# Kernel tuning notes

Hardware: AMD Instinct MI355X
Metric: run time of the kernel (lower is better)

The kernel has to match this reference:

```python
import jax, jax.numpy as jnp
import numpy as np

N_CH = 62
F_DIM = 16
T_DIM = 32
B_DIM = 256
N_NODES = B_DIM * N_CH  # 15872
E_DIM = 200000
SEQ = T_DIM * F_DIM  # 512


def setup_inputs() -> dict:
    key = jax.random.key(0)
    ks = iter(jax.random.split(key, 40))
    s = 0.05
    inp = {}
    inp['x'] = jax.random.normal(next(ks), (N_NODES, F_DIM, T_DIM), dtype=jnp.float32)
    inp['edge_index'] = jax.random.randint(next(ks), (T_DIM, 2, E_DIM), 0, N_NODES, dtype=jnp.int64)
    inp['edge_weight'] = jax.random.uniform(next(ks), (T_DIM, E_DIM), dtype=jnp.float32)
    inp['batch'] = jax.random.randint(next(ks), (T_DIM, N_NODES), 0, B_DIM, dtype=jnp.int64)
    # ChebConv params (K=2): lins have no bias, single bias added at end
    for p in ['c1', 'c2']:
        inp[p + '_w0'] = jax.random.normal(next(ks), (F_DIM, F_DIM), dtype=jnp.float32) * s
        inp[p + '_w1'] = jax.random.normal(next(ks), (F_DIM, F_DIM), dtype=jnp.float32) * s
        inp[p + '_b'] = jnp.zeros((F_DIM,), jnp.float32)
    # LSTM params (torch gate order i,f,g,o); fold b_ih+b_hh into one bias
    for name, i_dim, h_dim in [('l1', N_CH, 64), ('l2', 64, 128), ('l3', 128, 256)]:
        inp[name + '_wih'] = jax.random.normal(next(ks), (4 * h_dim, i_dim), dtype=jnp.float32) * s
        inp[name + '_whh'] = jax.random.normal(next(ks), (4 * h_dim, h_dim), dtype=jnp.float32) * s
        inp[name + '_b'] = jnp.zeros((4 * h_dim,), jnp.float32)
    # MLP head
    for name, i_dim, o_dim in [('fc1', SEQ * 256, 256), ('fc2', 256, 128), ('fc3', 128, 64), ('fc4', 64, 4)]:
        inp[name + '_w'] = jax.random.normal(next(ks), (i_dim, o_dim), dtype=jnp.float32) * s
        inp[name + '_b'] = jnp.zeros((o_dim,), jnp.float32)
    return inp


def _cheb(x, src, dst, w, w0, w1, b):
    # PyG ChebConv K=2, sym norm, lambda_max=2: Tx1 = -D^{-1/2} A D^{-1/2} x
    n = x.shape[0]
    deg = jax.ops.segment_sum(w, src, num_segments=n)
    dinv = jnp.where(deg > 0, jax.lax.rsqrt(deg), 0.0)
    norm = -dinv[src] * w * dinv[dst]
    tx1 = jax.ops.segment_sum(norm[:, None] * x[src], dst, num_segments=n)
    return x @ w0 + tx1 @ w1 + b


def _lstm(x, wih, whh, b):
    # x: [B, S, I] -> [B, S, H], batch_first, zero init state
    bsz, _, _ = x.shape
    h_dim = whh.shape[1]
    xg = x @ wih.T + b  # precompute input gates [B, S, 4H]
    def step(carry, xt):
        h, c = carry
        g = xt + h @ whh.T
        i, f, gg, o = jnp.split(g, 4, axis=-1)
        c = jax.nn.sigmoid(f) * c + jax.nn.sigmoid(i) * jnp.tanh(gg)
        h = jax.nn.sigmoid(o) * jnp.tanh(c)
        return (h, c), h
    h0 = jnp.zeros((bsz, h_dim), x.dtype)
    _, hs = jax.lax.scan(step, (h0, h0), jnp.swapaxes(xg, 0, 1))
    return jnp.swapaxes(hs, 0, 1)


def reference(x, edge_index, edge_weight, batch,
              c1_w0, c1_w1, c1_b, c2_w0, c2_w1, c2_b,
              l1_wih, l1_whh, l1_b, l2_wih, l2_whh, l2_b, l3_wih, l3_whh, l3_b,
              fc1_w, fc1_b, fc2_w, fc2_b, fc3_w, fc3_b, fc4_w, fc4_b):
    def per_t(xt, ei, w):
        h = _cheb(xt, ei[0], ei[1], w, c1_w0, c1_w1, c1_b)
        h = jax.nn.leaky_relu(h, 0.01)
        return _cheb(h, ei[0], ei[1], w, c2_w0, c2_w1, c2_b)
    xt_first = jnp.moveaxis(x, -1, 0)  # [T, N, F]
    h = jax.vmap(per_t)(xt_first, edge_index, edge_weight)  # [T, N, F]
    xc = jnp.moveaxis(h, 0, -1)  # [N, F, T]
    xc = xc.reshape(B_DIM, N_CH, F_DIM, T_DIM)
    xc = jnp.transpose(xc, (0, 3, 2, 1))  # [B, T, F, 62]
    xc = xc.reshape(B_DIM, T_DIM * F_DIM, N_CH)  # [B, S, 62]
    h = _lstm(xc, l1_wih, l1_whh, l1_b)
    h = _lstm(h, l2_wih, l2_whh, l2_b)
    h = _lstm(h, l3_wih, l3_whh, l3_b)
    z = h.reshape(B_DIM, -1)  # [B, S*256]
    z = jax.nn.relu(z @ fc1_w + fc1_b)
    z = jax.nn.relu(z @ fc2_w + fc2_b)
    z = jax.nn.relu(z @ fc3_w + fc3_b)
    return z @ fc4_w + fc4_b
```

## Files before the change

kernel.cpp:

```cpp
#include <hip/hip_runtime.h>
#include <cstdint>
#include <cstddef>


#define T_DIM 32
#define F_DIMC 16
#define NNODE 15872
#define EDGES 200000
#define BATCH 256
#define SEQL 512
#define TN (T_DIM * NNODE)
#define TE (T_DIM * EDGES)

typedef unsigned short ushortT;
typedef __bf16 bf16_t;
typedef bf16_t bf16x8 __attribute__((ext_vector_type(8)));
typedef float f32x4 __attribute__((ext_vector_type(4)));

__device__ __forceinline__ ushortT f2bf(float f) {
  union { float f; unsigned u; } v; v.f = f;
  unsigned u = v.u;
  u += 0x7fffu + ((u >> 16) & 1u);
  return (ushortT)(u >> 16);
}
__device__ __forceinline__ float fsig(float x) { return 1.0f / (1.0f + __expf(-x)); }
__device__ __forceinline__ float ftanh(float x) {
  float e = __expf(2.0f * x);
  return 1.0f - 2.0f / (e + 1.0f);
}
#define PIN(v) asm volatile("" : "+v"(v))

__device__ __forceinline__ void bar_sync() {
  asm volatile("s_waitcnt lgkmcnt(0)\n\ts_barrier" ::: "memory");
  __builtin_amdgcn_sched_barrier(0);
}

__global__ void k_wprep(const float* __restrict__ w1i, const float* __restrict__ w1h,
                        const float* __restrict__ w2i, const float* __restrict__ w2h,
                        const float* __restrict__ w3i, const float* __restrict__ w3h,
                        ushortT* __restrict__ Wcat) {
  int id = blockIdx.x * 256 + threadIdx.x;
  if (id >= 524288) return;
  float v;
  if (id < 32768) {
    int g = id >> 7, k = id & 127;
    v = (k < 62) ? w1i[g * 62 + k] : ((k >= 64) ? w1h[g * 64 + (k - 64)] : 0.0f);
  } else if (id < 131072) {
    int j = id - 32768; int g = j / 192, k = j % 192;
    v = (k < 64) ? w2i[g * 64 + k] : w2h[g * 128 + (k - 64)];
  } else {
    int j = id - 131072; int g = j / 384, k = j % 384;
    v = (k < 128) ? w3i[g * 128 + k] : w3h[g * 256 + (k - 128)];
  }
  Wcat[id] = f2bf(v);
}

__global__ void k_transpose(const float* __restrict__ x, float* __restrict__ xt) {
  __shared__ float s[528];
  int n = blockIdx.x;
  int tid = threadIdx.x;
  for (int i = tid; i < 512; i += 256) {
    s[(i >> 5) * 33 + (i & 31)] = x[(size_t)n * 512 + i];
  }
  __syncthreads();
  for (int i = tid; i < 512; i += 256) {
    int t = i >> 4, f = i & 15;
    xt[((size_t)t * NNODE + n) * 16 + f] = s[f * 33 + t];
  }
}

__global__ void k_degcount(const int* __restrict__ ei, const float* __restrict__ ew,
                           float* __restrict__ deg, int* __restrict__ counts) {
  int id = blockIdx.x * 256 + threadIdx.x;
  if (id >= TE) return;
  int t = id / EDGES, e = id % EDGES;
  int src = ei[(2 * t) * EDGES + e];
  int dst = ei[(2 * t + 1) * EDGES + e];
  atomicAdd(&deg[t * NNODE + src], ew[id]);
  atomicAdd(&counts[t * NNODE + dst], 1);
}

__global__ void k_scanA(const int* __restrict__ counts, int* __restrict__ offs,
                        int* __restrict__ ctot, float* __restrict__ deg) {
  __shared__ int s[256];
  int tid = threadIdx.x;
  int gid = blockIdx.x * 256 + tid;
  float d = deg[gid];
  int v = counts[gid];
  s[tid] = v; __syncthreads();
  for (int off = 1; off < 256; off <<= 1) {
    int x = (tid >= off) ? s[tid - off] : 0;
    __syncthreads();
    s[tid] += x;
    __syncthreads();
  }
  offs[gid] = s[tid] - v;
  if (tid == 255) ctot[blockIdx.x] = s[255];
  deg[gid] = (d > 0.0f) ? rsqrtf(d) : 0.0f;
}

__global__ void k_scanB(const int* __restrict__ ctot, int* __restrict__ cbase) {
  __shared__ int s[256];
  int tid = threadIdx.x;
  int carry = 0;
  for (int c = 0; c < 8; ++c) {
    int i = c * 256 + tid;
    int v = (i < 1984) ? ctot[i] : 0;
    s[tid] = v; __syncthreads();
    for (int off = 1; off < 256; off <<= 1) {
      int x = (tid >= off) ? s[tid - off] : 0;
      __syncthreads();
      s[tid] += x;
      __syncthreads();
    }
    if (i < 1984) cbase[i] = carry + s[tid] - v;
    int tot = s[255];
    __syncthreads();
    carry += tot;
  }
}

__global__ void k_fill(const int* __restrict__ ei, const float* __restrict__ ew,
                       const float* __restrict__ dinv, const int* __restrict__ offs,
                       const int* __restrict__ cbase, int* __restrict__ fillc,
                       int* __restrict__ csrs, float* __restrict__ csrn) {
  int id = blockIdx.x * 256 + threadIdx.x;
  if (id >= TE) return;
  int t = id / EDGES, e = id % EDGES;
  int src = ei[(2 * t) * EDGES + e];
  int dst = ei[(2 * t + 1) * EDGES + e];
  int idx = t * NNODE + dst;
  int pos = offs[idx] + cbase[idx >> 8] + atomicAdd(&fillc[idx], 1);
  csrs[pos] = src;
  csrn[pos] = -dinv[t * NNODE + src] * ew[id] * dinv[idx];
}

__device__ __forceinline__ void fma4(float4& a, float sc, const float4 b) {
  a.x += sc * b.x; a.y += sc * b.y; a.z += sc * b.z; a.w += sc * b.w;
}

__global__ void k_gc(const float* __restrict__ in, const int* __restrict__ offs,
                     const int* __restrict__ cbase,
                     const int* __restrict__ csrs, const float* __restrict__ csrn,
                     const float* __restrict__ w0, const float* __restrict__ w1,
                     const float* __restrict__ bias, float* __restrict__ outF,
                     ushortT* __restrict__ outX, int mode) {
  __shared__ float sw0[256], sw1[256], sb[16];
  int tid = threadIdx.x;
  sw0[tid] = w0[tid];
  sw1[tid] = w1[tid];
  if (tid < 16) sb[tid] = bias[tid];
  __syncthreads();
  int idx = blockIdx.x * 256 + tid;
  if (idx >= TN) return;
  int t = idx / NNODE, n = idx % NNODE;
  const float4* rowp = (const float4*)(in + (size_t)idx * 16);
  float4 x0 = rowp[0], x1 = rowp[1], x2 = rowp[2], x3 = rowp[3];
  float4 a0 = {0, 0, 0, 0}, a1 = {0, 0, 0, 0}, a2 = {0, 0, 0, 0}, a3 = {0, 0, 0, 0};
  int beg = offs[idx] + cbase[idx >> 8];
  int end = (idx == TN - 1) ? TE : offs[idx + 1] + cbase[(idx + 1) >> 8];
  const float* base = in + (size_t)t * NNODE * 16;
  for (int p2 = beg; p2 < end; ++p2) {
    int s = csrs[p2];
    float nr = csrn[p2];
    const float4* rp = (const float4*)(base + (size_t)s * 16);
    fma4(a0, nr, rp[0]); fma4(a1, nr, rp[1]); fma4(a2, nr, rp[2]); fma4(a3, nr, rp[3]);
  }
  float xr[16], ar[16];
  *(float4*)&xr[0] = x0; *(float4*)&xr[4] = x1; *(float4*)&xr[8] = x2; *(float4*)&xr[12] = x3;
  *(float4*)&ar[0] = a0; *(float4*)&ar[4] = a1; *(float4*)&ar[8] = a2; *(float4*)&ar[12] = a3;
  float o[16];
#pragma unroll
  for (int j = 0; j < 16; ++j) o[j] = sb[j];
#pragma unroll
  for (int k = 0; k < 16; ++k) {
    float xv = xr[k], av = ar[k];
#pragma unroll
    for (int j = 0; j < 16; ++j) o[j] += xv * sw0[k * 16 + j] + av * sw1[k * 16 + j];
  }
  if (mode == 0) {
#pragma unroll
    for (int j = 0; j < 16; ++j) o[j] = (o[j] > 0.0f) ? o[j] : 0.01f * o[j];
    float4* op = (float4*)(outF + (size_t)idx * 16);
    op[0] = *(float4*)&o[0]; op[1] = *(float4*)&o[4];
    op[2] = *(float4*)&o[8]; op[3] = *(float4*)&o[12];
  } else {
    int bb = n / 62, ch = n % 62;
#pragma unroll
    for (int j = 0; j < 16; ++j)
      outX[((size_t)(bb * 512 + t * 16 + j)) * 64 + ch] = f2bf(o[j]);
    if (ch < 2) {
#pragma unroll
      for (int j = 0; j < 16; ++j)
        outX[((size_t)(bb * 512 + t * 16 + j)) * 64 + 62 + ch] = 0;
    }
  }
}

__global__ __launch_bounds__(512, 1) void k_lstm(const ushortT* __restrict__ xc,
                                                 const ushortT* __restrict__ Wcat,
                                                 const float* __restrict__ b1g,
                                                 const float* __restrict__ b2g,
                                                 const float* __restrict__ b3g,
                                                 ushortT* __restrict__ zbuf,
                                                 uint32_t* __restrict__ h2x,
                                                 uint32_t* __restrict__ xbuf) {
  __shared__ ushortT X1[2][16 * 72];
  __shared__ ushortT H1[2][16 * 72];
  __shared__ ushortT H2[2][16 * 136];
  __shared__ ushortT HS[2][16 * 136];
  __shared__ ushortT PS[2][16 * 136];
  __shared__ ushortT H2S[2][16 * 136];
  int tid = threadIdx.x;
  int wv = tid >> 6, lane = tid & 63;
  int col = lane & 15, koff = (lane >> 4) * 8, m = lane & 15;
  int bx = blockIdx.x;

  if (bx < 16) {
    int g = bx;
    int bg = g * 16;
    const ushortT* W1 = Wcat;
    const ushortT* W2 = Wcat + 32768;

    bf16x8 w1r[4][4];
    if (wv < 4) {
#pragma unroll
      for (int q = 0; q < 4; ++q)
#pragma unroll
        for (int k = 0; k < 4; ++k) {
          w1r[q][k] = *reinterpret_cast<const bf16x8*>(
              &W1[(size_t)(q * 64 + wv * 16 + col) * 128 + k * 32 + koff]);
          PIN(w1r[q][k]);
        }
    }
    bf16x8 w2r[4][6];
#pragma unroll
    for (int q = 0; q < 4; ++q)
#pragma unroll
      for (int k = 0; k < 6; ++k) {
        w2r[q][k] = *reinterpret_cast<const bf16x8*>(
            &W2[(size_t)(q * 128 + wv * 16 + col) * 192 + k * 32 + koff]);
        PIN(w2r[q][k]);
      }
    float b1v[4] = {0, 0, 0, 0}, b2v[4];
    if (wv < 4) {
#pragma unroll
      for (int q = 0; q < 4; ++q) b1v[q] = b1g[q * 64 + wv * 16 + col];
    }
#pragma unroll
    for (int q = 0; q < 4; ++q) b2v[q] = b2g[q * 128 + wv * 16 + col];

    float c1r[4] = {0, 0, 0, 0};
    float c2r[4] = {0, 0, 0, 0};

    for (int i = tid; i < 2 * 16 * 72; i += 512) { X1[0][i] = 0; H1[0][i] = 0; }
    for (int i = tid; i < 2 * 16 * 136; i += 512) H2[0][i] = 0;
    __syncthreads();
    uint4 xreg = {0, 0, 0, 0};
    {
      int tid2 = tid - 256;
      if (tid2 >= 0 && tid2 < 128) {
        int mm = tid2 >> 3, jj = (tid2 & 7) * 8;
        *(uint4*)&X1[0][mm * 72 + jj] =
            *(const uint4*)&xc[((size_t)(bg + mm) * 512 + 0) * 64 + jj];
        xreg = *(const uint4*)&xc[((size_t)(bg + mm) * 512 + 1) * 64 + jj];
      }
    }
    __syncthreads();

    uint32_t* h2g = h2x + (size_t)g * 512 * 2048;

    for (int t = 0; t < 512; ++t) {
      int pr = t & 1, pw = 1 - pr;
      if (wv < 4) {
        f32x4 acc[4] = {};
#pragma unroll
        for (int kt = 0; kt < 4; ++kt) {
          const ushortT* ap = (kt < 2) ? &X1[pr][m * 72 + kt * 32 + koff]
                                       : &H1[pr][m * 72 + (kt - 2) * 32 + koff];
          bf16x8 a = *reinterpret_cast<const bf16x8*>(ap);
#pragma unroll
          for (int q = 0; q < 4; ++q)
            acc[q] = __builtin_amdgcn_mfma_f32_16x16x32_bf16(a, w1r[q][kt], acc[q], 0, 0, 0);
        }
#pragma unroll
        for (int r = 0; r < 4; ++r) {
          int row = (lane >> 4) * 4 + r;
          int lc = wv * 16 + col;
          float gi = acc[0][r] + b1v[0];
          float gf = acc[1][r] + b1v[1];
          float gg = acc[2][r] + b1v[2];
          float go = acc[3][r] + b1v[3];
          float c = fsig(gf) * c1r[r] + fsig(gi) * ftanh(gg);
          float h = fsig(go) * ftanh(c);
          c1r[r] = c;
          H1[pw][row * 72 + lc] = f2bf(h);
        }
      } else {
        int tid2 = tid - 256;
        if (tid2 < 128) {
          int mm = tid2 >> 3, jj = (tid2 & 7) * 8;
          if (t + 1 < 512)
            *(uint4*)&X1[pw][mm * 72 + jj] = xreg;
          int tf = (t + 2 < 512) ? t + 2 : 511;
          xreg = *(const uint4*)&xc[((size_t)(bg + mm) * 512 + tf) * 64 + jj];
        }
      }
      bar_sync();
      {
        f32x4 acc[4] = {};
#pragma unroll
        for (int kt = 0; kt < 6; ++kt) {
          const ushortT* ap = (kt < 2) ? &H1[pw][m * 72 + kt * 32 + koff]
                                       : &H2[pr][m * 136 + (kt - 2) * 32 + koff];
          bf16x8 a = *reinterpret_cast<const bf16x8*>(ap);
#pragma unroll
          for (int q = 0; q < 4; ++q)
            acc[q] = __builtin_amdgcn_mfma_f32_16x16x32_bf16(a, w2r[q][kt], acc[q], 0, 0, 0);
        }
        uint32_t tag = ((uint32_t)(t + 1)) << 16;
#pragma unroll
        for (int r = 0; r < 4; ++r) {
          int row = (lane >> 4) * 4 + r;
          int lc = wv * 16 + col;
          float gi = acc[0][r] + b2v[0];
          float gf = acc[1][r] + b2v[1];
          float gg = acc[2][r] + b2v[2];
          float go = acc[3][r] + b2v[3];
          float c = fsig(gf) * c2r[r] + fsig(gi) * ftanh(gg);
          float h = fsig(go) * ftanh(c);
          c2r[r] = c;
          ushortT hb = f2bf(h);
          H2[pw][row * 136 + lc] = hb;
          __hip_atomic_store(&h2g[(size_t)t * 2048 + row * 128 + lc], tag | hb,
                             __ATOMIC_RELAXED, __HIP_MEMORY_SCOPE_AGENT);
        }
      }
      bar_sync();
    }
  } else {
    int bxx = bx - 16;
    int s = (bxx >> 3) & 1;
    int g = (bxx & 7) | ((bxx >> 4) << 3);
    int ps = 1 - s;
    int bg = g * 16;
    const ushortT* W3 = Wcat + 131072;

    bf16x8 wH[4][4], wO[4][4], wP[4][4];
#pragma unroll
    for (int q = 0; q < 4; ++q) {
      const ushortT* rw = &W3[(size_t)(q * 256 + s * 128 + wv * 16 + col) * 384];
#pragma unroll
      for (int j = 0; j < 4; ++j) {
        wH[q][j] = *reinterpret_cast<const bf16x8*>(&rw[j * 32 + koff]);
        wO[q][j] = *reinterpret_cast<const bf16x8*>(&rw[(4 + s * 4 + j) * 32 + koff]);
        wP[q][j] = *reinterpret_cast<const bf16x8*>(&rw[(4 + ps * 4 + j) * 32 + koff]);
        PIN(wH[q][j]); PIN(wO[q][j]); PIN(wP[q][j]);
      }
    }
    float b3v[4];
#pragma unroll
    for (int q = 0; q < 4; ++q) b3v[q] = b3g[q * 256 + s * 128 + wv * 16 + col];

    float c3r[4] = {0, 0, 0, 0};

    for (int i = tid; i < 2 * 16 * 136; i += 512) HS[0][i] = 0;
    __syncthreads();

    uint32_t* myslot = xbuf + (((size_t)g * 2 + s) * 2) * 2048;
    const uint32_t* pslot = xbuf + (((size_t)g * 2 + ps) * 2) * 2048;
    const uint32_t* h2g = h2x + (size_t)g * 512 * 2048;

    int prow = tid >> 5, pc0 = (tid & 31) * 4;

    {
      const uint32_t* hp = h2g + prow * 128 + pc0;
      uint32_t u0 = __hip_atomic_load(hp + 0, __ATOMIC_RELAXED, __HIP_MEMORY_SCOPE_AGENT);
      uint32_t u1 = __hip_atomic_load(hp + 1, __ATOMIC_RELAXED, __HIP_MEMORY_SCOPE_AGENT);
      uint32_t u2 = __hip_atomic_load(hp + 2, __ATOMIC_RELAXED, __HIP_MEMORY_SCOPE_AGENT);
      uint32_t u3 = __hip_atomic_load(hp + 3, __ATOMIC_RELAXED, __HIP_MEMORY_SCOPE_AGENT);
      for (;;) {
        bool ok = ((u0 >> 16) == 1u) & ((u1 >> 16) == 1u) &
                  ((u2 >> 16) == 1u) & ((u3 >> 16) == 1u);
        if (ok) break;
        u0 = __hip_atomic_load(hp + 0, __ATOMIC_RELAXED, __HIP_MEMORY_SCOPE_AGENT);
        u1 = __hip_atomic_load(hp + 1, __ATOMIC_RELAXED, __HIP_MEMORY_SCOPE_AGENT);
        u2 = __hip_atomic_load(hp + 2, __ATOMIC_RELAXED, __HIP_MEMORY_SCOPE_AGENT);
        u3 = __hip_atomic_load(hp + 3, __ATOMIC_RELAXED, __HIP_MEMORY_SCOPE_AGENT);
      }
      H2S[0][prow * 136 + pc0 + 0] = (ushortT)(u0 & 0xffffu);
      H2S[0][prow * 136 + pc0 + 1] = (ushortT)(u1 & 0xffffu);
      H2S[0][prow * 136 + pc0 + 2] = (ushortT)(u2 & 0xffffu);
      H2S[0][prow * 136 + pc0 + 3] = (ushortT)(u3 & 0xffffu);
    }
    __syncthreads();

    for (int t = 0; t < 512; ++t) {
      int prt = t & 1, pw = 1 - prt;
      const uint32_t* pb = pslot + (size_t)prt * 2048 + prow * 128 + pc0;
      uint32_t v0 = 0, v1 = 0, v2 = 0, v3 = 0;
      if (t > 0) {
        v0 = __hip_atomic_load(pb + 0, __ATOMIC_RELAXED, __HIP_MEMORY_SCOPE_AGENT);
        v1 = __hip_atomic_load(pb + 1, __ATOMIC_RELAXED, __HIP_MEMORY_SCOPE_AGENT);
        v2 = __hip_atomic_load(pb + 2, __ATOMIC_RELAXED, __HIP_MEMORY_SCOPE_AGENT);
        v3 = __hip_atomic_load(pb + 3, __ATOMIC_RELAXED, __HIP_MEMORY_SCOPE_AGENT);
      }
      const uint32_t* hp = h2g + (size_t)(t + 1) * 2048 + prow * 128 + pc0;
      uint32_t u0 = 0, u1 = 0, u2 = 0, u3 = 0;
      if (t < 511) {
        u0 = __hip_atomic_load(hp + 0, __ATOMIC_RELAXED, __HIP_MEMORY_SCOPE_AGENT);
        u1 = __hip_atomic_load(hp + 1, __ATOMIC_RELAXED, __HIP_MEMORY_SCOPE_AGENT);
        u2 = __hip_atomic_load(hp + 2, __ATOMIC_RELAXED, __HIP_MEMORY_SCOPE_AGENT);
        u3 = __hip_atomic_load(hp + 3, __ATOMIC_RELAXED, __HIP_MEMORY_SCOPE_AGENT);
      }
      __builtin_amdgcn_sched_barrier(0);
      f32x4 acc[4] = {};
#pragma unroll
      for (int kt = 0; kt < 4; ++kt) {
        bf16x8 a = *reinterpret_cast<const bf16x8*>(&H2S[prt][m * 136 + kt * 32 + koff]);
#pragma unroll
        for (int q = 0; q < 4; ++q)
          acc[q] = __builtin_amdgcn_mfma_f32_16x16x32_bf16(a, wH[q][kt], acc[q], 0, 0, 0);
      }
      if (t > 0) {
#pragma unroll
        for (int j = 0; j < 4; ++j) {
          bf16x8 a = *reinterpret_cast<const bf16x8*>(&HS[prt][m * 136 + j * 32 + koff]);
#pragma unroll
          for (int q = 0; q < 4; ++q)
            acc[q] = __builtin_amdgcn_mfma_f32_16x16x32_bf16(a, wO[q][j], acc[q], 0, 0, 0);
        }
        {
          uint32_t want = (uint32_t)t;
          while (((v0 >> 16) != want) | ((v1 >> 16) != want) |
                 ((v2 >> 16) != want) | ((v3 >> 16) != want)) {
            v0 = __hip_atomic_load(pb + 0, __ATOMIC_RELAXED, __HIP_MEMORY_SCOPE_AGENT);
            v1 = __hip_atomic_load(pb + 1, __ATOMIC_RELAXED, __HIP_MEMORY_SCOPE_AGENT);
            v2 = __hip_atomic_load(pb + 2, __ATOMIC_RELAXED, __HIP_MEMORY_SCOPE_AGENT);
            v3 = __hip_atomic_load(pb + 3, __ATOMIC_RELAXED, __HIP_MEMORY_SCOPE_AGENT);
          }
          PS[prt][prow * 136 + pc0 + 0] = (ushortT)(v0 & 0xffffu);
          PS[prt][prow * 136 + pc0 + 1] = (ushortT)(v1 & 0xffffu);
          PS[prt][prow * 136 + pc0 + 2] = (ushortT)(v2 & 0xffffu);
          PS[prt][prow * 136 + pc0 + 3] = (ushortT)(v3 & 0xffffu);
        }
        bar_sync();
#pragma unroll
        for (int j = 0; j < 4; ++j) {
          bf16x8 a = *reinterpret_cast<const bf16x8*>(&PS[prt][m * 136 + j * 32 + koff]);
#pragma unroll
          for (int q = 0; q < 4; ++q)
            acc[q] = __builtin_amdgcn_mfma_f32_16x16x32_bf16(a, wP[q][j], acc[q], 0, 0, 0);
        }
      }
      if (t < 511) {
        uint32_t want = (uint32_t)(t + 2);
        while (((u0 >> 16) != want) | ((u1 >> 16) != want) |
               ((u2 >> 16) != want) | ((u3 >> 16) != want)) {
          u0 = __hip_atomic_load(hp + 0, __ATOMIC_RELAXED, __HIP_MEMORY_SCOPE_AGENT);
          u1 = __hip_atomic_load(hp + 1, __ATOMIC_RELAXED, __HIP_MEMORY_SCOPE_AGENT);
          u2 = __hip_atomic_load(hp + 2, __ATOMIC_RELAXED, __HIP_MEMORY_SCOPE_AGENT);
          u3 = __hip_atomic_load(hp + 3, __ATOMIC_RELAXED, __HIP_MEMORY_SCOPE_AGENT);
        }
        H2S[pw][prow * 136 + pc0 + 0] = (ushortT)(u0 & 0xffffu);
        H2S[pw][prow * 136 + pc0 + 1] = (ushortT)(u1 & 0xffffu);
        H2S[pw][prow * 136 + pc0 + 2] = (ushortT)(u2 & 0xffffu);
        H2S[pw][prow * 136 + pc0 + 3] = (ushortT)(u3 & 0xffffu);
      }
      uint32_t* mw = myslot + (size_t)((t + 1) & 1) * 2048;
      ushortT hbs[4];
#pragma unroll
      for (int r = 0; r < 4; ++r) {
        int row = (lane >> 4) * 4 + r;
        int lc = wv * 16 + col;
        float gi = acc[0][r] + b3v[0];
        float gf = acc[1][r] + b3v[1];
        float gg = acc[2][r] + b3v[2];
        float go = acc[3][r] + b3v[3];
        float c = fsig(gf) * c3r[r] + fsig(gi) * ftanh(gg);
        float h = fsig(go) * ftanh(c);
        c3r[r] = c;
        hbs[r] = f2bf(h);
        __hip_atomic_store(mw + row * 128 + lc, ((uint32_t)(t + 1) << 16) | hbs[r],
                           __ATOMIC_RELAXED, __HIP_MEMORY_SCOPE_AGENT);
      }
      asm volatile("s_waitcnt vmcnt(0)" ::: "memory");
      __builtin_amdgcn_sched_barrier(0);
#pragma unroll
      for (int r = 0; r < 4; ++r) {
        int row = (lane >> 4) * 4 + r;
        int lc = wv * 16 + col;
        HS[pw][row * 136 + lc] = hbs[r];
        zbuf[((size_t)(bg + row) * 512 + t) * 256 + s * 128 + lc] = hbs[r];
      }
      bar_sync();
    }
  }
}

__global__ __launch_bounds__(256) void k_fc1(const ushortT* __restrict__ zbuf,
                                             const float* __restrict__ w,
                                             float* __restrict__ part) {
  __shared__ ushortT As[256 * 40];
  __shared__ ushortT Bs[64 * 40];
  int tid = threadIdx.x;
  int kb = blockIdx.x;
  int nb = blockIdx.y;
  int wv = tid >> 6, lane = tid & 63;
  int col = lane & 15, koff = (lane >> 4) * 8;
  int k0base = kb * 2048;
  f32x4 acc[4][4] = {};
  for (int kt = 0; kt < 64; ++kt) {
    int k0 = k0base + kt * 32;
    {
      const uint4* src = (const uint4*)(zbuf + (size_t)tid * 131072 + k0);
      uint4* dst = (uint4*)(As + tid * 40);
      dst[0] = src[0]; dst[1] = src[1]; dst[2] = src[2]; dst[3] = src[3];
    }
    {
      int kk = tid >> 3, j0 = (tid & 7) * 8;
      const float* srcw = w + (size_t)(k0 + kk) * 256 + nb * 64 + j0;
#pragma unroll
      for (int jj = 0; jj < 8; ++jj) Bs[(j0 + jj) * 40 + kk] = f2bf(srcw[jj]);
    }
    __syncthreads();
    bf16x8 bfr[4];
#pragma unroll
    for (int nt = 0; nt < 4; ++nt)
      bfr[nt] = *reinterpret_cast<const bf16x8*>(&Bs[(nt * 16 + col) * 40 + koff]);
#pragma unroll
    for (int mt = 0; mt < 4; ++mt) {
      bf16x8 afr = *reinterpret_cast<const bf16x8*>(&As[(wv * 64 + mt * 16 + col) * 40 + koff]);
#pragma unroll
      for (int nt = 0; nt < 4; ++nt)
        acc[mt][nt] = __builtin_amdgcn_mfma_f32_16x16x32_bf16(afr, bfr[nt], acc[mt][nt], 0, 0, 0);
    }
    __syncthreads();
  }
#pragma unroll
  for (int mt = 0; mt < 4; ++mt)
#pragma unroll
    for (int nt = 0; nt < 4; ++nt)
#pragma unroll
      for (int r = 0; r < 4; ++r) {
        int m = wv * 64 + mt * 16 + (lane >> 4) * 4 + r;
        int n = nb * 64 + nt * 16 + col;
        part[(size_t)kb * 65536 + m * 256 + n] = acc[mt][nt][r];
      }
}

__global__ void k_fc1red(const float* __restrict__ part, const float* __restrict__ b,
                         float* __restrict__ out) {
  int id4 = blockIdx.x * 256 + threadIdx.x;
  if (id4 >= 16384) return;
  float4 s = {0.0f, 0.0f, 0.0f, 0.0f};
  for (int kb = 0; kb < 64; ++kb) {
    float4 v = *(const float4*)&part[(size_t)kb * 65536 + id4 * 4];
    s.x += v.x; s.y += v.y; s.z += v.z; s.w += v.w;
  }
  int n0 = (id4 * 4) & 255;
  s.x = fmaxf(s.x + b[n0 + 0], 0.0f);
  s.y = fmaxf(s.y + b[n0 + 1], 0.0f);
  s.z = fmaxf(s.z + b[n0 + 2], 0.0f);
  s.w = fmaxf(s.w + b[n0 + 3], 0.0f);
  *(float4*)&out[id4 * 4] = s;
}

__global__ void k_fcv(const float* __restrict__ in, const float* __restrict__ w,
                      const float* __restrict__ b, float* __restrict__ out,
                      int K, int Nn, int doRelu) {
  int id = blockIdx.x * 256 + threadIdx.x;
  int m = id / Nn, n = id % Nn;
  float s = b[n];
  for (int k = 0; k < K; ++k) s += in[m * K + k] * w[k * Nn + n];
  if (doRelu) s = fmaxf(s, 0.0f);
  out[id] = s;
}

extern "C" void kernel_launch(void* const* d_in, const int* in_sizes, int n_in,
                              void* d_out, int out_size, void* d_ws, size_t ws_size,
                              hipStream_t stream) {
  (void)in_sizes; (void)n_in; (void)out_size; (void)ws_size;
  const float* x    = (const float*)d_in[0];
  const int* ei     = (const int*)d_in[1];
  const float* ew   = (const float*)d_in[2];
  const float* c1w0 = (const float*)d_in[4];
  const float* c1w1 = (const float*)d_in[5];
  const float* c1b  = (const float*)d_in[6];
  const float* c2w0 = (const float*)d_in[7];
  const float* c2w1 = (const float*)d_in[8];
  const float* c2b  = (const float*)d_in[9];
  const float* l1wi = (const float*)d_in[10];
  const float* l1wh = (const float*)d_in[11];
  const float* l1b  = (const float*)d_in[12];
  const float* l2wi = (const float*)d_in[13];
  const float* l2wh = (const float*)d_in[14];
  const float* l2b  = (const float*)d_in[15];
  const float* l3wi = (const float*)d_in[16];
  const float* l3wh = (const float*)d_in[17];
  const float* l3b  = (const float*)d_in[18];
  const float* fc1w = (const float*)d_in[19];
  const float* fc1b = (const float*)d_in[20];
  const float* fc2w = (const float*)d_in[21];
  const float* fc2b = (const float*)d_in[22];
  const float* fc3w = (const float*)d_in[23];
  const float* fc3b = (const float*)d_in[24];
  const float* fc4w = (const float*)d_in[25];
  const float* fc4b = (const float*)d_in[26];
  float* out = (float*)d_out;

  char* p = (char*)d_ws;
  auto alloc = [&](size_t bytes) { void* r = (void*)p; p += (bytes + 255) & ~(size_t)255; return r; };
  float* xt      = (float*)alloc(32505856);
  float* h1buf   = (float*)alloc(32505856);
  float* dinv    = (float*)alloc(2031616);
  int* counts    = (int*)alloc(2031616);
  int* offs      = (int*)alloc(2031616);
  int* fillc     = (int*)alloc(2031616);
  int* ctot      = (int*)alloc(8192);
  int* cbase     = (int*)alloc(8192);
  int* csrs      = (int*)alloc(25600000);
  float* csrn    = (float*)alloc(25600000);
  ushortT* xc    = (ushortT*)alloc(16777216);
  ushortT* Wcat  = (ushortT*)alloc(1048576);
  ushortT* zbuf  = (ushortT*)alloc(67108864);
  float* part    = (float*)alloc(16777216);
  float* fo1     = (float*)alloc(262144);
  float* fo2     = (float*)alloc(131072);
  float* fo3     = (float*)alloc(65536);
  uint32_t* xbuf = (uint32_t*)alloc(524288);
  uint32_t* h2x = (uint32_t*)xt;

  hipMemsetAsync(dinv, 0, 2031616, stream);
  hipMemsetAsync(counts, 0, 2031616, stream);
  hipMemsetAsync(fillc, 0, 2031616, stream);

  k_wprep<<<2048, 256, 0, stream>>>(l1wi, l1wh, l2wi, l2wh, l3wi, l3wh, Wcat);
  k_transpose<<<15872, 256, 0, stream>>>(x, xt);
  k_degcount<<<25000, 256, 0, stream>>>(ei, ew, dinv, counts);
  k_scanA<<<1984, 256, 0, stream>>>(counts, offs, ctot, dinv);
  k_scanB<<<1, 256, 0, stream>>>(ctot, cbase);
  k_fill<<<25000, 256, 0, stream>>>(ei, ew, dinv, offs, cbase, fillc, csrs, csrn);
  k_gc<<<1984, 256, 0, stream>>>(xt, offs, cbase, csrs, csrn, c1w0, c1w1, c1b, h1buf, nullptr, 0);
  k_gc<<<1984, 256, 0, stream>>>(h1buf, offs, cbase, csrs, csrn, c2w0, c2w1, c2b, nullptr, xc, 1);
  hipMemsetAsync(h2x, 0, 67108864, stream);
  k_lstm<<<48, 512, 0, stream>>>(xc, Wcat, l1b, l2b, l3b, zbuf, h2x, xbuf);
  k_fc1<<<dim3(64, 4), 256, 0, stream>>>(zbuf, fc1w, part);
  k_fc1red<<<64, 256, 0, stream>>>(part, fc1b, fo1);
  k_fcv<<<128, 256, 0, stream>>>(fo1, fc2w, fc2b, fo2, 256, 128, 1);
  k_fcv<<<64, 256, 0, stream>>>(fo2, fc3w, fc3b, fo3, 128, 64, 1);
  k_fcv<<<4, 256, 0, stream>>>(fo3, fc4w, fc4b, out, 64, 4, 0);
}
```

Before: 3.606 ms.

## Build per-timestep degree and count histograms in LDS, recording per-edge rank

Replaces the global-atomic degree/count kernel with one 1024-thread block per timestep that accumulates degree and in-degree counts in shared memory (about 127KB of LDS). Each edge's slot within its destination bucket is recorded as a rank, so the CSR fill no longer needs a global atomic counter, and the three memsets go away. The cost is that only 32 blocks run the histogram, which limits parallelism across the GPU's many CUs. The rank array reuses the h1buf scratch buffer.

```diff
diff --git a/kernel.cpp b/kernel.cpp
--- a/kernel.cpp
+++ b/kernel.cpp
@@ -69,15 +69,35 @@
   }
 }
 
-__global__ void k_degcount(const int* __restrict__ ei, const float* __restrict__ ew,
-                           float* __restrict__ deg, int* __restrict__ counts) {
-  int id = blockIdx.x * 256 + threadIdx.x;
-  if (id >= TE) return;
-  int t = id / EDGES, e = id % EDGES;
-  int src = ei[(2 * t) * EDGES + e];
-  int dst = ei[(2 * t + 1) * EDGES + e];
-  atomicAdd(&deg[t * NNODE + src], ew[id]);
-  atomicAdd(&counts[t * NNODE + dst], 1);
+__global__ __launch_bounds__(1024, 1) void k_hist(const int* __restrict__ ei,
+                                                  const float* __restrict__ ew,
+                                                  float* __restrict__ deg,
+                                                  int* __restrict__ counts,
+                                                  int* __restrict__ rank) {
+  __shared__ float sdeg[NNODE];
+  __shared__ int scnt[NNODE];
+  int t = blockIdx.x;
+  int tid = threadIdx.x;
+  for (int i = tid; i < NNODE; i += 1024) { sdeg[i] = 0.0f; scnt[i] = 0; }
+  __syncthreads();
+  const int* srcp = ei + (size_t)(2 * t) * EDGES;
+  const int* dstp = ei + (size_t)(2 * t + 1) * EDGES;
+  const float* ewp = ew + (size_t)t * EDGES;
+  int* rankp = rank + (size_t)t * EDGES;
+  for (int e = tid; e < EDGES; e += 1024) {
+    int src = srcp[e];
+    int dst = dstp[e];
+    float w = ewp[e];
+    atomicAdd(&sdeg[src], w);
+    rankp[e] = atomicAdd(&scnt[dst], 1);
+  }
+  __syncthreads();
+  float* degp = deg + (size_t)t * NNODE;
+  int* cntp = counts + (size_t)t * NNODE;
+  for (int i = tid; i < NNODE; i += 1024) {
+    degp[i] = sdeg[i];
+    cntp[i] = scnt[i];
+  }
 }
 
 __global__ void k_scanA(const int* __restrict__ counts, int* __restrict__ offs,
@@ -120,17 +140,17 @@
   }
 }
 
-__global__ void k_fill(const int* __restrict__ ei, const float* __restrict__ ew,
-                       const float* __restrict__ dinv, const int* __restrict__ offs,
-                       const int* __restrict__ cbase, int* __restrict__ fillc,
-                       int* __restrict__ csrs, float* __restrict__ csrn) {
+__global__ void k_fill2(const int* __restrict__ ei, const float* __restrict__ ew,
+                        const float* __restrict__ dinv, const int* __restrict__ offs,
+                        const int* __restrict__ cbase, const int* __restrict__ rank,
+                        int* __restrict__ csrs, float* __restrict__ csrn) {
   int id = blockIdx.x * 256 + threadIdx.x;
   if (id >= TE) return;
   int t = id / EDGES, e = id % EDGES;
-  int src = ei[(2 * t) * EDGES + e];
-  int dst = ei[(2 * t + 1) * EDGES + e];
+  int src = ei[(size_t)(2 * t) * EDGES + e];
+  int dst = ei[(size_t)(2 * t + 1) * EDGES + e];
   int idx = t * NNODE + dst;
-  int pos = offs[idx] + cbase[idx >> 8] + atomicAdd(&fillc[idx], 1);
+  int pos = offs[idx] + cbase[idx >> 8] + rank[id];
   csrs[pos] = src;
   csrn[pos] = -dinv[t * NNODE + src] * ew[id] * dinv[idx];
 }
@@ -629,18 +649,17 @@
   float* fo2     = (float*)alloc(131072);
   float* fo3     = (float*)alloc(65536);
   uint32_t* xbuf = (uint32_t*)alloc(524288);
+  (void)fillc;
+  int* rank = (int*)h1buf;
   uint32_t* h2x = (uint32_t*)xt;
 
-  hipMemsetAsync(dinv, 0, 2031616, stream);
-  hipMemsetAsync(counts, 0, 2031616, stream);
-  hipMemsetAsync(fillc, 0, 2031616, stream);
 
   k_wprep<<<2048, 256, 0, stream>>>(l1wi, l1wh, l2wi, l2wh, l3wi, l3wh, Wcat);
   k_transpose<<<15872, 256, 0, stream>>>(x, xt);
-  k_degcount<<<25000, 256, 0, stream>>>(ei, ew, dinv, counts);
+  k_hist<<<32, 1024, 0, stream>>>(ei, ew, dinv, counts, rank);
   k_scanA<<<1984, 256, 0, stream>>>(counts, offs, ctot, dinv);
   k_scanB<<<1, 256, 0, stream>>>(ctot, cbase);
-  k_fill<<<25000, 256, 0, stream>>>(ei, ew, dinv, offs, cbase, fillc, csrs, csrn);
+  k_fill2<<<25000, 256, 0, stream>>>(ei, ew, dinv, offs, cbase, rank, csrs, csrn);
   k_gc<<<1984, 256, 0, stream>>>(xt, offs, cbase, csrs, csrn, c1w0, c1w1, c1b, h1buf, nullptr, 0);
   k_gc<<<1984, 256, 0, stream>>>(h1buf, offs, cbase, csrs, csrn, c2w0, c2w1, c2b, nullptr, xc, 1);
   hipMemsetAsync(h2x, 0, 67108864, stream);
```

After: 3.189 ms, median of 2. 1.13x faster.
